# Optimization experiments

Measured on AMD Instinct MI355X. Metric: run time of the kernel, lower is better.

Reference implementation:

```python
import jax, jax.numpy as jnp
import numpy as np

TEMP = 11.313708498984761  # sqrt(head_dim=128)

def setup_inputs() -> dict:
    key = jax.random.key(0)
    kq, kk, kv, km = jax.random.split(key, 4)
    B, H, S, D = 2, 16, 2048, 128
    q = jax.random.normal(kq, (B, H, S, D), dtype=jnp.float32)
    k = jax.random.normal(kk, (B, H, S, D), dtype=jnp.float32)
    v = jax.random.normal(kv, (B, H, S, D), dtype=jnp.float32)
    mask = jax.random.randint(km, (B, 1, S, S), 0, 2, dtype=jnp.int32)
    return {"q": q, "k": k, "v": v, "mask": mask}

def reference(q, k, v, mask):
    # atten = (q / temp) @ k^T  -> [B,H,S,S]
    atten = jnp.einsum("bhsd,bhtd->bhst", q / TEMP, k)
    maskf = mask.astype(atten.dtype)
    # torch masked_fill_(mask.bool(), 1e-9): positions where mask != 0 get 1e-9
    atten = jnp.where(mask.astype(bool), jnp.asarray(1e-9, atten.dtype), atten)
    atten = jax.nn.softmax(atten, axis=-1)
    # then multiply by mask (zeros out mask==0 positions)
    atten = atten * maskf
    # dropout: eval mode (identity) for a deterministic correctness baseline
    out = jnp.einsum("bhst,bhtd->bhsd", atten, v)
    return (out, atten)
```

## Files before the change

kernel.cpp:

```cpp
#include <hip/hip_runtime.h>
#include <stdint.h>

#define B_ 2
#define H_ 16
#define S_ 2048
#define D_ 128

typedef float f32x4 __attribute__((ext_vector_type(4)));
typedef float f32x16 __attribute__((ext_vector_type(16)));
typedef short bf16x8 __attribute__((ext_vector_type(8)));
typedef unsigned short u16x4 __attribute__((ext_vector_type(4)));
typedef int i32x4 __attribute__((ext_vector_type(4)));

__device__ __forceinline__ unsigned short f2bf(float x){
  union { float f; uint32_t u; } c; c.f = x;
  uint32_t u = c.u;
  uint32_t r = (u + 0x7FFFu + ((u >> 16) & 1u)) >> 16;
  return (unsigned short)r;
}

__device__ __forceinline__ void gload_lds16(const void* g, void* l){
  __builtin_amdgcn_global_load_lds(
      (const __attribute__((address_space(1))) unsigned int*)g,
      (__attribute__((address_space(3))) unsigned int*)l, 16, 0, 0);
}

__global__ void prep_kernel(const float* __restrict__ k, const float* __restrict__ v,
                            const int* __restrict__ mask,
                            unsigned short* __restrict__ KB, unsigned short* __restrict__ VT,
                            unsigned long long* __restrict__ bits){
  __shared__ float tile[64][73];
  const int blk = blockIdx.x;
  const int tid = threadIdx.x;
  if (blk < 8192){
    size_t i = (size_t)blk * 256 + tid;
    f32x4 val = __builtin_nontemporal_load(&((const f32x4*)k)[i]);
    u16x4 o; o[0]=f2bf(val.x); o[1]=f2bf(val.y); o[2]=f2bf(val.z); o[3]=f2bf(val.w);
    __builtin_nontemporal_store(o, &((u16x4*)KB)[i]);
  } else if (blk < 10240){
    int b2 = blk - 8192;
    int bh = b2 >> 6;
    int ts = (b2 >> 1) & 31;
    int dsec = b2 & 1;
    int t0 = ts*64, d0 = dsec*64;
    const float* vb = v + ((size_t)bh*S_ + t0)*D_ + d0;
    #pragma unroll
    for (int i=0;i<4;++i){
      int fi = i*256 + tid;
      int r = fi >> 4;
      int c4 = (fi & 15) * 4;
      f32x4 val = __builtin_nontemporal_load((const f32x4*)(vb + (size_t)r*D_ + c4));
      tile[r][c4+0]=val.x; tile[r][c4+1]=val.y; tile[r][c4+2]=val.z; tile[r][c4+3]=val.w;
    }
    __syncthreads();
    unsigned short* ob = VT + ((size_t)bh*D_ + d0)*S_ + t0;
    #pragma unroll
    for (int i=0;i<4;++i){
      int ui = i*256 + tid;
      int dr = ui >> 4;
      int tc = (ui & 15) * 4;
      u16x4 o;
      o[0] = f2bf(tile[tc+0][dr]);
      o[1] = f2bf(tile[tc+1][dr]);
      o[2] = f2bf(tile[tc+2][dr]);
      o[3] = f2bf(tile[tc+3][dr]);
      __builtin_nontemporal_store(o, (u16x4*)(ob + (size_t)dr*S_ + tc));
    }
  } else {
    int row = blk - 10240;
    const int* mrow = mask + (size_t)row*S_;
    int w = tid >> 6;
    int lane = tid & 63;
    #pragma unroll
    for (int i=0;i<8;++i){
      int t = i*256 + tid;
      unsigned long long bm = __ballot(__builtin_nontemporal_load(&mrow[t]) != 0);
      if (lane == 0) bits[(size_t)row*32 + i*4 + w] = bm;
    }
  }
}

__launch_bounds__(512, 4)
__global__ void fused_kernel(const float* __restrict__ q,
                             const unsigned long long* __restrict__ bits,
                             const unsigned short* __restrict__ KB,
                             const unsigned short* __restrict__ VT,
                             float* __restrict__ outp,
                             float* __restrict__ atten)
{
  __shared__ __align__(16) unsigned char Ksm[2][16384];
  __shared__ __align__(16) unsigned char Vsm[2][16384];
  __shared__ float lred[8][32];
  __shared__ float csm[128];
  const int tid = threadIdx.x;
  const int lane = tid & 63;
  const int w = tid >> 6;
  const int l32 = lane & 31;
  const int lh = lane >> 5;

  const int orig = blockIdx.x;
  const int blk = (orig & 7) * 64 + (orig >> 3);
  const int bh = blk >> 4;
  const int qt = blk & 15;
  const int b = bh >> 4;
  const int s0 = qt * 128;
  const int r = w >> 1;
  const int cQ = w & 1;
  const int qrow = s0 + 32*r + l32;

  const float QS = 1.4426950408889634f / 11.313708498984761f;

  bf16x8 qf[8];
  {
    const float* qp = q + ((size_t)bh*S_ + qrow)*D_ + 8*lh;
    #pragma unroll
    for (int m=0; m<8; ++m){
      f32x4 a0 = __builtin_nontemporal_load((const f32x4*)(qp + 16*m));
      f32x4 a1 = __builtin_nontemporal_load((const f32x4*)(qp + 16*m + 4));
      bf16x8 f;
      f[0]=(short)f2bf(a0.x*QS); f[1]=(short)f2bf(a0.y*QS);
      f[2]=(short)f2bf(a0.z*QS); f[3]=(short)f2bf(a0.w*QS);
      f[4]=(short)f2bf(a1.x*QS); f[5]=(short)f2bf(a1.y*QS);
      f[6]=(short)f2bf(a1.z*QS); f[7]=(short)f2bf(a1.w*QS);
      qf[m] = f;
    }
  }

  float lsum = 0.f;

  const unsigned char* Kgb = (const unsigned char*)(KB + (size_t)bh*S_*D_);
  const unsigned char* Vgb = (const unsigned char*)(VT + (size_t)bh*D_*S_);
  const unsigned long long* bitsb = bits + (size_t)b*S_*32 + (size_t)qrow*32;

  uint32_t koff[2], voff[2];
  int kbase[2];
  {
    int lq = lane >> 4, ls = lane & 15;
    #pragma unroll
    for (int i=0;i<2;++i){
      int c = 2*w + i;
      kbase[i] = c*1024;
      int rr = c*4 + lq;
      int ss = ls ^ (rr & 15);
      koff[i] = (uint32_t)(rr*256 + ss*16);
      int d  = rr*2 + (ss>>3);
      int ts = ss & 7;
      voff[i] = (uint32_t)(d*(S_*2) + ts*16);
    }
  }

  unsigned long long mbn = bitsb[0];
  #pragma unroll
  for (int i=0;i<2;++i)
    gload_lds16(Kgb + koff[i], &Ksm[0][kbase[i]]);

  int cur = 0;
  for (int it=0; it<32; ++it){
    asm volatile("s_waitcnt vmcnt(0)" ::: "memory");
    __builtin_amdgcn_sched_barrier(0);
    __builtin_amdgcn_s_barrier();
    __builtin_amdgcn_sched_barrier(0);

    unsigned long long mb = mbn;
    if (it+1 < 32){
      mbn = bitsb[it+1];
      const unsigned char* Kp = Kgb + (size_t)(it+1)*16384;
      #pragma unroll
      for (int i=0;i<2;++i)
        gload_lds16(Kp + koff[i], &Ksm[cur^1][kbase[i]]);
      __builtin_amdgcn_sched_barrier(0);
    }

    f32x16 Sacc;
    #pragma unroll
    for (int e=0;e<16;++e) Sacc[e] = 0.f;
    const int trow = 32*cQ + l32;
    const unsigned char* kb = &Ksm[cur][trow*256];
    const int txr = trow & 15;
    __builtin_amdgcn_s_setprio(1);
    #pragma unroll
    for (int m=0; m<8; ++m){
      int slot = (2*m + lh) ^ txr;
      bf16x8 kf = *(const bf16x8*)(kb + (slot<<4));
      Sacc = __builtin_amdgcn_mfma_f32_32x32x16_bf16(kf, qf[m], Sacc, 0,0,0);
    }
    __builtin_amdgcn_s_setprio(0);

    uint32_t mw = (uint32_t)(mb >> (32*cQ + 4*lh));
    #pragma unroll
    for (int reg=0; reg<16; ++reg){
      const int tb = (reg&3) + 8*(reg>>2);
      float x = ((mw >> tb) & 1u) ? 0.f : Sacc[reg];
      lsum += __builtin_amdgcn_exp2f(x);
    }
    cur ^= 1;
  }

  lsum += __shfl_xor(lsum, 32);
  if (lane < 32) lred[w][l32] = lsum;
  __syncthreads();
  if (tid < 128){
    int rr = tid >> 5;
    csm[tid] = 1.0f / (lred[2*rr][tid&31] + lred[2*rr+1][tid&31]);
  }

  unsigned long long* bitlds = (unsigned long long*)&Ksm[0][0];
  {
    const i32x4* bsrc = (const i32x4*)(bits + ((size_t)b*S_ + s0)*32);
    i32x4* bdst = (i32x4*)bitlds;
    #pragma unroll
    for (int i=0;i<4;++i)
      bdst[i*512 + tid] = bsrc[i*512 + tid];
  }
  unsigned long long mb2n = bitsb[0];
  #pragma unroll
  for (int i=0;i<2;++i)
    gload_lds16(Vgb + voff[i], &Vsm[0][kbase[i]]);
  __syncthreads();

  f32x16 Wacc[2];
  #pragma unroll
  for (int n=0;n<2;++n)
    #pragma unroll
    for (int e=0;e<16;++e) Wacc[n][e] = 0.f;

  f32x4* abase = (f32x4*)(atten + ((size_t)bh*S_ + s0)*S_);
  const int aword = tid >> 4;
  const int ash = (tid & 15)*4;

  cur = 0;
  for (int it=0; it<32; ++it){
    unsigned long long mb = mb2n;
    if (it+1 < 32){
      mb2n = bitsb[it+1];
      const unsigned char* Vp = Vgb + (size_t)(it+1)*128;
      #pragma unroll
      for (int i=0;i<2;++i)
        gload_lds16(Vp + voff[i], &Vsm[cur^1][kbase[i]]);
      __builtin_amdgcn_sched_barrier(0);
    }

    unsigned long long ms = mb >> (8*lh);
    uint32_t mlo = (uint32_t)ms, mhi = (uint32_t)(ms >> 32);
    #pragma unroll
    for (int m2=0; m2<4; ++m2){
      uint32_t bt = ((m2 < 2 ? mlo : mhi) >> (16*(m2&1))) & 0xFFu;
      union { bf16x8 v; uint32_t u[4]; } pk;
      #pragma unroll
      for (int j2=0; j2<4; ++j2){
        pk.u[j2] = (((bt>>(2*j2))&1u) ? 0x3F80u : 0u)
                 | (((bt>>(2*j2+1))&1u) ? 0x3F800000u : 0u);
      }
      __builtin_amdgcn_s_setprio(1);
      #pragma unroll
      for (int n=0; n<2; ++n){
        const int dd = 32*(2*cQ + n) + l32;
        int slot = ((((dd&1)<<3) | (2*m2 + lh)) ^ ((dd>>1)&15));
        bf16x8 vf = *(const bf16x8*)(&Vsm[cur][(dd>>1)*256 + (slot<<4)]);
        Wacc[n] = __builtin_amdgcn_mfma_f32_32x32x16_bf16(pk.v, vf, Wacc[n], 0,0,0);
      }
      __builtin_amdgcn_s_setprio(0);
    }

    #pragma unroll
    for (int sub=0; sub<4; ++sub){
      int j = 4*it + sub;
      float c = csm[j];
      unsigned long long wv = bitlds[j*32 + aword];
      uint32_t nib = (uint32_t)(wv >> ash) & 0xFu;
      f32x4 o = { (nib&1u)?c:0.f, (nib&2u)?c:0.f, (nib&4u)?c:0.f, (nib&8u)?c:0.f };
      __builtin_nontemporal_store(o, &abase[j*512 + tid]);
    }

    if (it+1 < 32){
      __builtin_amdgcn_sched_barrier(0);
      asm volatile("s_waitcnt vmcnt(4)" ::: "memory");
      __builtin_amdgcn_sched_barrier(0);
      __builtin_amdgcn_s_barrier();
      __builtin_amdgcn_sched_barrier(0);
    }
    cur ^= 1;
  }

  #pragma unroll
  for (int reg=0; reg<16; ++reg){
    int crow = (reg&3) + 8*(reg>>2) + 4*lh;
    float cv = csm[32*r + crow];
    int row = s0 + 32*r + crow;
    #pragma unroll
    for (int n=0; n<2; ++n){
      const int dd = 32*(2*cQ + n) + l32;
      __builtin_nontemporal_store(cv*Wacc[n][reg],
                                  &outp[((size_t)bh*S_ + row)*D_ + dd]);
    }
  }
}

extern "C" void kernel_launch(void* const* d_in, const int* in_sizes, int n_in,
                              void* d_out, int out_size, void* d_ws, size_t ws_size,
                              hipStream_t stream){
  const float* q = (const float*)d_in[0];
  const float* k = (const float*)d_in[1];
  const float* v = (const float*)d_in[2];
  const int* mask = (const int*)d_in[3];
  float* outp = (float*)d_out;
  float* atten = outp + (size_t)B_*H_*S_*D_;

  unsigned short* KB = (unsigned short*)d_ws;
  unsigned short* VT = KB + (size_t)B_*H_*S_*D_;
  unsigned long long* bits = (unsigned long long*)(VT + (size_t)B_*H_*S_*D_);

  hipLaunchKernelGGL(prep_kernel,  dim3(14336), dim3(256), 0, stream, k, v, mask, KB, VT, bits);
  hipLaunchKernelGGL(fused_kernel, dim3(512),   dim3(512), 0, stream, q, bits, KB, VT, outp, atten);
}
```

Before: 261.3 us.

## Read V directly from global in PV phase and drop LDS staging and barriers

The second pass no longer double-buffers V tiles through LDS with async global-to-LDS loads, waitcnts and block barriers. Each lane now loads its bf16x8 V fragment straight from global memory, relying on L2 for reuse. Mask bits come from the LDS copy instead of a global prefetch, and the attention-matrix stores are moved to the start of each iteration. The aim is to let the bandwidth-heavy attention writes stream without barrier stalls and to free 32KB of LDS, at the cost of redundant, less coalesced V reads from cache across waves.

```diff
diff --git a/kernel.cpp b/kernel.cpp
--- a/kernel.cpp
+++ b/kernel.cpp
@@ -89,7 +89,6 @@
                              float* __restrict__ atten)
 {
   __shared__ __align__(16) unsigned char Ksm[2][16384];
-  __shared__ __align__(16) unsigned char Vsm[2][16384];
   __shared__ float lred[8][32];
   __shared__ float csm[128];
   const int tid = threadIdx.x;
@@ -129,10 +128,10 @@
   float lsum = 0.f;
 
   const unsigned char* Kgb = (const unsigned char*)(KB + (size_t)bh*S_*D_);
-  const unsigned char* Vgb = (const unsigned char*)(VT + (size_t)bh*D_*S_);
+  const unsigned short* Vg = VT + (size_t)bh*D_*S_;
   const unsigned long long* bitsb = bits + (size_t)b*S_*32 + (size_t)qrow*32;
 
-  uint32_t koff[2], voff[2];
+  uint32_t koff[2];
   int kbase[2];
   {
     int lq = lane >> 4, ls = lane & 15;
@@ -143,9 +142,6 @@
       int rr = c*4 + lq;
       int ss = ls ^ (rr & 15);
       koff[i] = (uint32_t)(rr*256 + ss*16);
-      int d  = rr*2 + (ss>>3);
-      int ts = ss & 7;
-      voff[i] = (uint32_t)(d*(S_*2) + ts*16);
     }
   }
 
@@ -212,10 +208,6 @@
     for (int i=0;i<4;++i)
       bdst[i*512 + tid] = bsrc[i*512 + tid];
   }
-  unsigned long long mb2n = bitsb[0];
-  #pragma unroll
-  for (int i=0;i<2;++i)
-    gload_lds16(Vgb + voff[i], &Vsm[0][kbase[i]]);
   __syncthreads();
 
   f32x16 Wacc[2];
@@ -227,19 +219,20 @@
   f32x4* abase = (f32x4*)(atten + ((size_t)bh*S_ + s0)*S_);
   const int aword = tid >> 4;
   const int ash = (tid & 15)*4;
-
-  cur = 0;
+  const int lr = 32*r + l32;
+
   for (int it=0; it<32; ++it){
-    unsigned long long mb = mb2n;
-    if (it+1 < 32){
-      mb2n = bitsb[it+1];
-      const unsigned char* Vp = Vgb + (size_t)(it+1)*128;
-      #pragma unroll
-      for (int i=0;i<2;++i)
-        gload_lds16(Vp + voff[i], &Vsm[cur^1][kbase[i]]);
-      __builtin_amdgcn_sched_barrier(0);
-    }
-
+    #pragma unroll
+    for (int sub=0; sub<4; ++sub){
+      int j = 4*it + sub;
+      float c = csm[j];
+      unsigned long long wv = bitlds[j*32 + aword];
+      uint32_t nib = (uint32_t)(wv >> ash) & 0xFu;
+      f32x4 o = { (nib&1u)?c:0.f, (nib&2u)?c:0.f, (nib&4u)?c:0.f, (nib&8u)?c:0.f };
+      __builtin_nontemporal_store(o, &abase[j*512 + tid]);
+    }
+
+    unsigned long long mb = bitlds[lr*32 + it];
     unsigned long long ms = mb >> (8*lh);
     uint32_t mlo = (uint32_t)ms, mhi = (uint32_t)(ms >> 32);
     #pragma unroll
@@ -251,35 +244,13 @@
         pk.u[j2] = (((bt>>(2*j2))&1u) ? 0x3F80u : 0u)
                  | (((bt>>(2*j2+1))&1u) ? 0x3F800000u : 0u);
       }
-      __builtin_amdgcn_s_setprio(1);
       #pragma unroll
       for (int n=0; n<2; ++n){
         const int dd = 32*(2*cQ + n) + l32;
-        int slot = ((((dd&1)<<3) | (2*m2 + lh)) ^ ((dd>>1)&15));
-        bf16x8 vf = *(const bf16x8*)(&Vsm[cur][(dd>>1)*256 + (slot<<4)]);
+        bf16x8 vf = *(const bf16x8*)(Vg + (size_t)dd*S_ + it*64 + m2*16 + lh*8);
         Wacc[n] = __builtin_amdgcn_mfma_f32_32x32x16_bf16(pk.v, vf, Wacc[n], 0,0,0);
       }
-      __builtin_amdgcn_s_setprio(0);
-    }
-
-    #pragma unroll
-    for (int sub=0; sub<4; ++sub){
-      int j = 4*it + sub;
-      float c = csm[j];
-      unsigned long long wv = bitlds[j*32 + aword];
-      uint32_t nib = (uint32_t)(wv >> ash) & 0xFu;
-      f32x4 o = { (nib&1u)?c:0.f, (nib&2u)?c:0.f, (nib&4u)?c:0.f, (nib&8u)?c:0.f };
-      __builtin_nontemporal_store(o, &abase[j*512 + tid]);
-    }
-
-    if (it+1 < 32){
-      __builtin_amdgcn_sched_barrier(0);
-      asm volatile("s_waitcnt vmcnt(4)" ::: "memory");
-      __builtin_amdgcn_sched_barrier(0);
-      __builtin_amdgcn_s_barrier();
-      __builtin_amdgcn_sched_barrier(0);
-    }
-    cur ^= 1;
+    }
   }
 
   #pragma unroll
```

Measured after the change: 280.5 us. +7.4%, slower.
